# Optimization experiments

Measured on AMD Instinct MI355X. Metric: run time of the kernel, lower is better.

Reference implementation:

```python
import jax, jax.numpy as jnp
import numpy as np

P = 126          # num_patients
EPS = 1e-6       # PCSL eps
BN_EPS = 1e-5    # torch BatchNorm1d default eps (eval mode: running_mean=0, running_var=1)
LAMBDA_PCSL = 50.0
LAMBDA_DANN = 0.5


def setup_inputs() -> dict:
    key = jax.random.key(0)
    ks = jax.random.split(key, 8)
    D, H1, H2 = 768, 256, 128
    inp = {
        "features": jax.random.normal(ks[0], (2048, 16, D), dtype=jnp.float32),
        "patient_ids": jax.random.randint(ks[1], (2048,), 0, P),
        "W1": jax.random.normal(ks[2], (D, H1), dtype=jnp.float32) / np.sqrt(D),
        "b1": jnp.zeros((H1,), jnp.float32),
        "g1": jnp.ones((H1,), jnp.float32),
        "be1": jnp.zeros((H1,), jnp.float32),
        "W2": jax.random.normal(ks[3], (H1, H2), dtype=jnp.float32) / np.sqrt(H1),
        "b2": jnp.zeros((H2,), jnp.float32),
        "g2": jnp.ones((H2,), jnp.float32),
        "be2": jnp.zeros((H2,), jnp.float32),
        "W3": jax.random.normal(ks[4], (H2, P), dtype=jnp.float32) / np.sqrt(H2),
        "b3": jnp.zeros((P,), jnp.float32),
    }
    return inp


@jax.custom_vjp
def grl(x):  # gradient reversal, lambda_=1.0 (forward identity)
    return x

def _grl_fwd(x):
    return x, None

def _grl_bwd(_, g):
    return (-g,)

grl.defvjp(_grl_fwd, _grl_bwd)


def _bn_eval(x, gamma, beta):
    # BatchNorm1d in eval mode with fresh running stats (mean=0, var=1)
    return x * (gamma / jnp.sqrt(1.0 + BN_EPS)) + beta


def reference(features, patient_ids, W1, b1, g1, be1, W2, b2, g2, be2, W3, b3):
    f = features.mean(axis=1)  # [B, D]

    # ---- PCSL: segment mean/variance + pairwise centroid distances ----
    counts = jax.ops.segment_sum(jnp.ones_like(f[:, 0]), patient_ids, num_segments=P)
    sums = jax.ops.segment_sum(f, patient_ids, num_segments=P)        # [P, D]
    present = counts > 0
    centroids = sums / jnp.maximum(counts, 1.0)[:, None]              # [P, D]
    within = jnp.sum((f - centroids[patient_ids]) ** 2)
    sq = jnp.sum(centroids ** 2, axis=-1)                              # [P]
    d2 = sq[:, None] + sq[None, :] - 2.0 * centroids @ centroids.T     # [P, P]
    pair_mask = present[:, None] & present[None, :]
    between = 0.5 * jnp.sum(jnp.where(pair_mask, d2, 0.0))             # sum over i<j (diag=0)
    loss_pcsl = within / (between + EPS)

    # ---- DANN: GRL + discriminator + CE over compacted patient ids ----
    # mapped id = rank of pid among present unique ids (matches torch.unique remap)
    mapped = jnp.cumsum(present.astype(jnp.int32))[patient_ids] - 1
    x = grl(f)
    h = jax.nn.relu(_bn_eval(x @ W1 + b1, g1, be1))
    h = jax.nn.relu(_bn_eval(h @ W2 + b2, g2, be2))
    logits = h @ W3 + b3                                               # [B, P]
    logp = jax.nn.log_softmax(logits, axis=-1)
    loss_dann = -jnp.mean(jnp.take_along_axis(logp, mapped[:, None], axis=-1))

    return LAMBDA_PCSL * loss_pcsl + LAMBDA_DANN * loss_dann
```

## Files before the change

kernel.cpp:

```cpp
#include <hip/hip_runtime.h>
#include <math.h>

#define B_ 2048
#define S_ 16
#define D_ 768
#define H1_ 256
#define H2_ 128
#define P_ 126

static constexpr float EPS = 1e-6f;
static constexpr float BN_EPS = 1e-5f;
static constexpr float L_PCSL = 50.0f;
static constexpr float L_DANN = 0.5f;

typedef __attribute__((ext_vector_type(8))) short bf16x8;
typedef __attribute__((ext_vector_type(4))) float f32x4;

__device__ inline unsigned short f2b(float x) {
    unsigned int u = __float_as_uint(x);
    unsigned int r = (u + 0x7fffu + ((u >> 16) & 1u)) >> 16;
    return (unsigned short)r;
}

__global__ __launch_bounds__(256) void k_cvt(const float* __restrict__ W1,
                                             const float* __restrict__ W2,
                                             const float* __restrict__ W3,
                                             unsigned short* __restrict__ W1T,
                                             unsigned short* __restrict__ W2T,
                                             unsigned short* __restrict__ W3T,
                                             const int* __restrict__ pid,
                                             int* __restrict__ mapped) {
    int b = blockIdx.x;
    int tid = threadIdx.x;
    if (b == 60) {
        __shared__ int hist[128];
        if (tid < 128) hist[tid] = 0;
        __syncthreads();
        for (int i = tid; i < B_; i += 256) atomicAdd(&hist[pid[i]], 1);
        __syncthreads();
        if (tid == 0) {
            int run = 0;
            for (int p = 0; p < P_; ++p) {
                mapped[p] = (hist[p] > 0) ? run : -1;
                if (hist[p] > 0) run++;
            }
        }
        return;
    }
    __shared__ float tile[64][65];
    const float* src; unsigned short* dst; int R, C, r0, c0;
    if (b < 48)      { src = W1; dst = W1T; R = 768; C = 256; int t = b;      r0 = (t >> 2) * 64; c0 = (t & 3) * 64; }
    else if (b < 56) { src = W2; dst = W2T; R = 256; C = 128; int t = b - 48; r0 = (t >> 1) * 64; c0 = (t & 1) * 64; }
    else             { src = W3; dst = W3T; R = 128; C = 126; int t = b - 56; r0 = (t >> 1) * 64; c0 = (t & 1) * 64; }
#pragma unroll
    for (int i = 0; i < 16; ++i) {
        int idx = tid + i * 256;
        int rr = idx >> 6, cc = idx & 63;
        tile[rr][cc] = (c0 + cc < C) ? src[(size_t)(r0 + rr) * C + c0 + cc] : 0.f;
    }
    __syncthreads();
#pragma unroll
    for (int i = 0; i < 16; ++i) {
        int idx = tid + i * 256;
        int rr = idx >> 6, cc = idx & 63;
        dst[(size_t)(c0 + rr) * R + r0 + cc] = f2b(tile[cc][rr]);
    }
}

__global__ __launch_bounds__(192) void k_mean(const float* __restrict__ feat,
                                              float* __restrict__ f,
                                              unsigned short* __restrict__ fbf) {
    int b = blockIdx.x;
    int t = threadIdx.x;
    const float4* src = (const float4*)(feat + (size_t)b * S_ * D_);
    float4 acc = make_float4(0.f, 0.f, 0.f, 0.f);
#pragma unroll
    for (int s = 0; s < S_; ++s) {
        float4 v = src[s * (D_ / 4) + t];
        acc.x += v.x; acc.y += v.y; acc.z += v.z; acc.w += v.w;
    }
    const float inv = 1.0f / (float)S_;
    acc.x *= inv; acc.y *= inv; acc.z *= inv; acc.w *= inv;
    ((float4*)(f + (size_t)b * D_))[t] = acc;
    ((ushort4*)(fbf + (size_t)b * D_))[t] =
        make_ushort4(f2b(acc.x), f2b(acc.y), f2b(acc.z), f2b(acc.w));
}

__global__ __launch_bounds__(192) void k_centroid(const float* __restrict__ f,
                                                  const int* __restrict__ pid,
                                                  float* __restrict__ colsum,
                                                  float* __restrict__ scal) {
    __shared__ int sid[B_];
    __shared__ int list[B_];
    __shared__ int s_cnt;
    __shared__ float wredA[3], wredB[3];
    int p = blockIdx.x;
    int t = threadIdx.x;
    for (int i = t; i < B_; i += 192) sid[i] = pid[i];
    __syncthreads();

    if (t < 64) {
        int total = 0;
        unsigned long long lt_mask = (t == 63) ? 0x7fffffffffffffffull
                                               : ((1ull << t) - 1ull);
#pragma unroll 4
        for (int r = 0; r < B_ / 64; ++r) {
            int b = r * 64 + t;
            bool m = (sid[b] == p);
            unsigned long long mask = __ballot(m);
            if (m) {
                int pos = total + (int)__popcll(mask & lt_mask);
                list[pos] = b;
            }
            total += (int)__popcll(mask);
        }
        if (t == 0) s_cnt = total;
    }
    __syncthreads();

    int cnt = s_cnt;
    float4 acc = make_float4(0.f, 0.f, 0.f, 0.f);
    float ssf = 0.f;
    int i = 0;
    for (; i + 4 <= cnt; i += 4) {
        int b0 = list[i], b1 = list[i + 1], b2 = list[i + 2], b3 = list[i + 3];
        float4 v0 = ((const float4*)(f + (size_t)b0 * D_))[t];
        float4 v1 = ((const float4*)(f + (size_t)b1 * D_))[t];
        float4 v2 = ((const float4*)(f + (size_t)b2 * D_))[t];
        float4 v3 = ((const float4*)(f + (size_t)b3 * D_))[t];
        acc.x += v0.x + v1.x + v2.x + v3.x;
        acc.y += v0.y + v1.y + v2.y + v3.y;
        acc.z += v0.z + v1.z + v2.z + v3.z;
        acc.w += v0.w + v1.w + v2.w + v3.w;
        ssf += v0.x * v0.x + v0.y * v0.y + v0.z * v0.z + v0.w * v0.w;
        ssf += v1.x * v1.x + v1.y * v1.y + v1.z * v1.z + v1.w * v1.w;
        ssf += v2.x * v2.x + v2.y * v2.y + v2.z * v2.z + v2.w * v2.w;
        ssf += v3.x * v3.x + v3.y * v3.y + v3.z * v3.z + v3.w * v3.w;
    }
    for (; i < cnt; ++i) {
        float4 v = ((const float4*)(f + (size_t)list[i] * D_))[t];
        acc.x += v.x; acc.y += v.y; acc.z += v.z; acc.w += v.w;
        ssf += v.x * v.x + v.y * v.y + v.z * v.z + v.w * v.w;
    }

    float invc = 1.0f / (float)(cnt > 0 ? cnt : 1);
    float4 c = make_float4(acc.x * invc, acc.y * invc, acc.z * invc, acc.w * invc);
    atomicAdd(&colsum[4 * t + 0], c.x);
    atomicAdd(&colsum[4 * t + 1], c.y);
    atomicAdd(&colsum[4 * t + 2], c.z);
    atomicAdd(&colsum[4 * t + 3], c.w);
    float ssc = c.x * c.x + c.y * c.y + c.z * c.z + c.w * c.w;
    for (int off = 32; off; off >>= 1) {
        ssf += __shfl_down(ssf, off, 64);
        ssc += __shfl_down(ssc, off, 64);
    }
    if ((t & 63) == 0) { wredA[t >> 6] = ssf; wredB[t >> 6] = ssc; }
    __syncthreads();
    if (t == 0) {
        float sumsq_rows = wredA[0] + wredA[1] + wredA[2];
        float sqp = wredB[0] + wredB[1] + wredB[2];
        atomicAdd(&scal[3], sumsq_rows);
        atomicAdd(&scal[4], (float)cnt * sqp);
        atomicAdd(&scal[5], sqp);
        atomicAdd(&scal[6], cnt > 0 ? 1.f : 0.f);
    }
}

__global__ __launch_bounds__(256) void k_mlp(const unsigned short* __restrict__ fbf,
                                             const unsigned short* __restrict__ W1T,
                                             const unsigned short* __restrict__ W2T,
                                             const unsigned short* __restrict__ W3T,
                                             const float* __restrict__ b1,
                                             const float* __restrict__ g1,
                                             const float* __restrict__ be1,
                                             const float* __restrict__ b2,
                                             const float* __restrict__ g2,
                                             const float* __restrict__ be2,
                                             const float* __restrict__ b3,
                                             const int* __restrict__ pid,
                                             const int* __restrict__ mapped,
                                             float* __restrict__ scal) {
    constexpr int LD1 = H1_ + 8;
    constexpr int LD2 = H2_ + 8;
    __shared__ unsigned short Hs[16 * LD1];
    __shared__ unsigned short H2s[16 * LD2];
    __shared__ float smax[4][16], ssum[4][16];
    __shared__ int spid[16];
    int tid = threadIdx.x;
    int w = tid >> 6, lane = tid & 63, lg = lane >> 4, li = lane & 15;
    int r0 = blockIdx.x * 16;
    if (tid < 16) spid[tid] = pid[r0 + tid];
    const float inv_bn = rsqrtf(1.0f + BN_EPS);

    f32x4 acc[4];
#pragma unroll
    for (int nf = 0; nf < 4; ++nf) acc[nf] = (f32x4){0.f, 0.f, 0.f, 0.f};
    const unsigned short* aptr = fbf + (size_t)(r0 + li) * D_ + lg * 8;
#pragma unroll 2
    for (int k0 = 0; k0 < D_; k0 += 32) {
        bf16x8 a8 = *(const bf16x8*)(aptr + k0);
#pragma unroll
        for (int nf = 0; nf < 4; ++nf) {
            bf16x8 b8 = *(const bf16x8*)(W1T + (size_t)(w * 64 + nf * 16 + li) * D_ + k0 + lg * 8);
            acc[nf] = __builtin_amdgcn_mfma_f32_16x16x32_bf16(a8, b8, acc[nf], 0, 0, 0);
        }
    }
#pragma unroll
    for (int nf = 0; nf < 4; ++nf) {
        int col = w * 64 + nf * 16 + li;
        float sc = g1[col] * inv_bn, bb = b1[col], bt = be1[col];
#pragma unroll
        for (int r = 0; r < 4; ++r) {
            int row = lg * 4 + r;
            float v = fmaxf((acc[nf][r] + bb) * sc + bt, 0.f);
            Hs[row * LD1 + col] = f2b(v);
        }
    }
    __syncthreads();

    f32x4 acc2[2];
    acc2[0] = (f32x4){0.f, 0.f, 0.f, 0.f};
    acc2[1] = (f32x4){0.f, 0.f, 0.f, 0.f};
#pragma unroll
    for (int ks = 0; ks < H1_ / 32; ++ks) {
        bf16x8 a8 = *(const bf16x8*)(Hs + li * LD1 + ks * 32 + lg * 8);
#pragma unroll
        for (int mf = 0; mf < 2; ++mf) {
            bf16x8 b8 = *(const bf16x8*)(W2T + (size_t)(w * 32 + mf * 16 + li) * H1_ + ks * 32 + lg * 8);
            acc2[mf] = __builtin_amdgcn_mfma_f32_16x16x32_bf16(a8, b8, acc2[mf], 0, 0, 0);
        }
    }
#pragma unroll
    for (int mf = 0; mf < 2; ++mf) {
        int col = w * 32 + mf * 16 + li;
        float sc = g2[col] * inv_bn, bb = b2[col], bt = be2[col];
#pragma unroll
        for (int r = 0; r < 4; ++r) {
            int row = lg * 4 + r;
            float v = fmaxf((acc2[mf][r] + bb) * sc + bt, 0.f);
            H2s[row * LD2 + col] = f2b(v);
        }
    }
    __syncthreads();

    f32x4 acc3[2];
    acc3[0] = (f32x4){0.f, 0.f, 0.f, 0.f};
    acc3[1] = (f32x4){0.f, 0.f, 0.f, 0.f};
#pragma unroll
    for (int ks = 0; ks < H2_ / 32; ++ks) {
        bf16x8 a8 = *(const bf16x8*)(H2s + li * LD2 + ks * 32 + lg * 8);
#pragma unroll
        for (int mf = 0; mf < 2; ++mf) {
            bf16x8 b8 = *(const bf16x8*)(W3T + (size_t)(w * 32 + mf * 16 + li) * H2_ + ks * 32 + lg * 8);
            acc3[mf] = __builtin_amdgcn_mfma_f32_16x16x32_bf16(a8, b8, acc3[mf], 0, 0, 0);
        }
    }
    int c0 = w * 32 + li, c1 = w * 32 + 16 + li;
    float bb0 = (c0 < P_) ? b3[c0] : 0.f;
    float bb1 = (c1 < P_) ? b3[c1] : 0.f;
    float lg0[4], lg1[4], m[4];
#pragma unroll
    for (int r = 0; r < 4; ++r) {
        lg0[r] = (c0 < P_) ? (acc3[0][r] + bb0) : -3.0e38f;
        lg1[r] = (c1 < P_) ? (acc3[1][r] + bb1) : -3.0e38f;
        m[r] = fmaxf(lg0[r], lg1[r]);
    }
#pragma unroll
    for (int off = 1; off < 16; off <<= 1)
#pragma unroll
        for (int r = 0; r < 4; ++r) m[r] = fmaxf(m[r], __shfl_xor(m[r], off, 64));
    if (li == 0) {
#pragma unroll
        for (int r = 0; r < 4; ++r) smax[w][lg * 4 + r] = m[r];
    }
    __syncthreads();
    float M[4], s[4];
#pragma unroll
    for (int r = 0; r < 4; ++r) {
        int row = lg * 4 + r;
        M[r] = fmaxf(fmaxf(smax[0][row], smax[1][row]), fmaxf(smax[2][row], smax[3][row]));
        s[r] = __expf(lg0[r] - M[r]) + __expf(lg1[r] - M[r]);
    }
#pragma unroll
    for (int off = 1; off < 16; off <<= 1)
#pragma unroll
        for (int r = 0; r < 4; ++r) s[r] += __shfl_xor(s[r], off, 64);
    if (li == 0) {
#pragma unroll
        for (int r = 0; r < 4; ++r) ssum[w][lg * 4 + r] = s[r];
    }
    __syncthreads();
    float part = 0.f;
#pragma unroll
    for (int r = 0; r < 4; ++r) {
        int row = lg * 4 + r;
        float se = ssum[0][row] + ssum[1][row] + ssum[2][row] + ssum[3][row];
        float lnse = M[r] + __logf(se);
        int mb = mapped[spid[row]];
        if (c0 == mb) part += lnse - lg0[r];
        if (c1 == mb) part += lnse - lg1[r];
    }
    for (int off = 32; off; off >>= 1) part += __shfl_down(part, off, 64);
    if (lane == 0) atomicAdd(&scal[2], part);
}

__global__ __launch_bounds__(256) void k_final(const float* __restrict__ colsum,
                                               const float* __restrict__ scal,
                                               float* __restrict__ out) {
    __shared__ float wred[4];
    int t = threadIdx.x;
    float acc = 0.f;
    for (int d = t; d < D_; d += 256) {
        float cs = colsum[d];
        acc += cs * cs;
    }
    for (int off = 32; off; off >>= 1) acc += __shfl_down(acc, off, 64);
    if ((t & 63) == 0) wred[t >> 6] = acc;
    __syncthreads();
    if (t == 0) {
        float B2 = wred[0] + wred[1] + wred[2] + wred[3];
        float within = scal[3] - scal[4];
        float between = scal[6] * scal[5] - B2;
        out[0] = L_PCSL * (within / (between + EPS)) + L_DANN * (scal[2] / (float)B_);
    }
}

extern "C" void kernel_launch(void* const* d_in, const int* in_sizes, int n_in,
                              void* d_out, int out_size, void* d_ws, size_t ws_size,
                              hipStream_t stream) {
    const float* feat = (const float*)d_in[0];
    const int* pid = (const int*)d_in[1];
    const float* W1 = (const float*)d_in[2];
    const float* b1 = (const float*)d_in[3];
    const float* g1 = (const float*)d_in[4];
    const float* be1 = (const float*)d_in[5];
    const float* W2 = (const float*)d_in[6];
    const float* b2 = (const float*)d_in[7];
    const float* g2 = (const float*)d_in[8];
    const float* be2 = (const float*)d_in[9];
    const float* W3 = (const float*)d_in[10];
    const float* b3 = (const float*)d_in[11];
    float* out = (float*)d_out;

    char* w = (char*)d_ws;
    float* colsum = (float*)w;
    float* scal = colsum + D_;
    int* mapped = (int*)(scal + 16);
    float* f = (float*)(mapped + 128);
    unsigned short* fbf = (unsigned short*)(f + (size_t)B_ * D_);
    unsigned short* W1T = fbf + (size_t)B_ * D_;
    unsigned short* W2T = W1T + (size_t)H1_ * D_;
    unsigned short* W3T = W2T + (size_t)H2_ * H1_;

    hipMemsetAsync(colsum, 0, (D_ + 16) * sizeof(float), stream);

    k_cvt<<<61, 256, 0, stream>>>(W1, W2, W3, W1T, W2T, W3T, pid, mapped);
    k_mean<<<B_, 192, 0, stream>>>(feat, f, fbf);
    k_centroid<<<P_, 192, 0, stream>>>(f, pid, colsum, scal);
    k_mlp<<<B_ / 16, 256, 0, stream>>>(fbf, W1T, W2T, W3T, b1, g1, be1,
                                       b2, g2, be2, b3, pid, mapped, scal);
    k_final<<<1, 256, 0, stream>>>(colsum, scal, out);
}
```

Baseline: 80.04 us.

## Fuse five kernels into two and drop fp32 mean buffer

Merges the weight-transpose kernel into the feature-mean kernel, and merges the centroid, MLP and final kernels into one launch that uses a last-block atomic counter to do the final reduction. The fp32 copy of the mean features is no longer written, and centroid statistics are read from the bf16 buffer instead. This cuts launch gaps and about half of the mean-output traffic. In exchange the PCSL statistics are computed from bf16-rounded features, which loses precision, and the MLP blocks use a larger shared-memory union, which may lower occupancy.

Result: faster. 76.06 us (-5.0%).

```diff
diff --git a/kernel.cpp b/kernel.cpp
--- a/kernel.cpp
+++ b/kernel.cpp
@@ -21,8 +21,17 @@
     unsigned int r = (u + 0x7fffu + ((u >> 16) & 1u)) >> 16;
     return (unsigned short)r;
 }
-
-__global__ __launch_bounds__(256) void k_cvt(const float* __restrict__ W1,
+__device__ inline float b2f(unsigned short u) {
+    return __uint_as_float((unsigned int)u << 16);
+}
+__device__ inline float4 ldrow(const unsigned short* __restrict__ fbf, int b, int t) {
+    ushort4 u = ((const ushort4*)(fbf + (size_t)b * D_))[t];
+    return make_float4(b2f(u.x), b2f(u.y), b2f(u.z), b2f(u.w));
+}
+
+__global__ __launch_bounds__(256) void k_pre(const float* __restrict__ feat,
+                                             unsigned short* __restrict__ fbf,
+                                             const float* __restrict__ W1,
                                              const float* __restrict__ W2,
                                              const float* __restrict__ W3,
                                              unsigned short* __restrict__ W1T,
@@ -30,298 +39,306 @@
                                              unsigned short* __restrict__ W3T,
                                              const int* __restrict__ pid,
                                              int* __restrict__ mapped) {
+    __shared__ union {
+        float tile[64][65];
+        int hist[128];
+    } sh;
     int b = blockIdx.x;
     int tid = threadIdx.x;
-    if (b == 60) {
-        __shared__ int hist[128];
-        if (tid < 128) hist[tid] = 0;
-        __syncthreads();
-        for (int i = tid; i < B_; i += 256) atomicAdd(&hist[pid[i]], 1);
+
+    if (b < B_) {
+        if (tid < 192) {
+            const float4* src = (const float4*)(feat + (size_t)b * S_ * D_);
+            float4 acc = make_float4(0.f, 0.f, 0.f, 0.f);
+#pragma unroll
+            for (int s = 0; s < S_; ++s) {
+                float4 v = src[s * (D_ / 4) + tid];
+                acc.x += v.x; acc.y += v.y; acc.z += v.z; acc.w += v.w;
+            }
+            const float inv = 1.0f / (float)S_;
+            acc.x *= inv; acc.y *= inv; acc.z *= inv; acc.w *= inv;
+            ((ushort4*)(fbf + (size_t)b * D_))[tid] =
+                make_ushort4(f2b(acc.x), f2b(acc.y), f2b(acc.z), f2b(acc.w));
+        }
+        return;
+    }
+    if (b == B_ + 60) {
+        if (tid < 128) sh.hist[tid] = 0;
+        __syncthreads();
+        for (int i = tid; i < B_; i += 256) atomicAdd(&sh.hist[pid[i]], 1);
         __syncthreads();
         if (tid == 0) {
             int run = 0;
             for (int p = 0; p < P_; ++p) {
-                mapped[p] = (hist[p] > 0) ? run : -1;
-                if (hist[p] > 0) run++;
+                mapped[p] = (sh.hist[p] > 0) ? run : -1;
+                if (sh.hist[p] > 0) run++;
             }
         }
         return;
     }
-    __shared__ float tile[64][65];
+    int bb = b - B_;
     const float* src; unsigned short* dst; int R, C, r0, c0;
-    if (b < 48)      { src = W1; dst = W1T; R = 768; C = 256; int t = b;      r0 = (t >> 2) * 64; c0 = (t & 3) * 64; }
-    else if (b < 56) { src = W2; dst = W2T; R = 256; C = 128; int t = b - 48; r0 = (t >> 1) * 64; c0 = (t & 1) * 64; }
-    else             { src = W3; dst = W3T; R = 128; C = 126; int t = b - 56; r0 = (t >> 1) * 64; c0 = (t & 1) * 64; }
+    if (bb < 48)      { src = W1; dst = W1T; R = 768; C = 256; int t = bb;      r0 = (t >> 2) * 64; c0 = (t & 3) * 64; }
+    else if (bb < 56) { src = W2; dst = W2T; R = 256; C = 128; int t = bb - 48; r0 = (t >> 1) * 64; c0 = (t & 1) * 64; }
+    else              { src = W3; dst = W3T; R = 128; C = 126; int t = bb - 56; r0 = (t >> 1) * 64; c0 = (t & 1) * 64; }
 #pragma unroll
     for (int i = 0; i < 16; ++i) {
         int idx = tid + i * 256;
         int rr = idx >> 6, cc = idx & 63;
-        tile[rr][cc] = (c0 + cc < C) ? src[(size_t)(r0 + rr) * C + c0 + cc] : 0.f;
+        sh.tile[rr][cc] = (c0 + cc < C) ? src[(size_t)(r0 + rr) * C + c0 + cc] : 0.f;
     }
     __syncthreads();
 #pragma unroll
     for (int i = 0; i < 16; ++i) {
         int idx = tid + i * 256;
         int rr = idx >> 6, cc = idx & 63;
-        dst[(size_t)(c0 + rr) * R + r0 + cc] = f2b(tile[cc][rr]);
-    }
-}
-
-__global__ __launch_bounds__(192) void k_mean(const float* __restrict__ feat,
-                                              float* __restrict__ f,
-                                              unsigned short* __restrict__ fbf) {
-    int b = blockIdx.x;
-    int t = threadIdx.x;
-    const float4* src = (const float4*)(feat + (size_t)b * S_ * D_);
-    float4 acc = make_float4(0.f, 0.f, 0.f, 0.f);
-#pragma unroll
-    for (int s = 0; s < S_; ++s) {
-        float4 v = src[s * (D_ / 4) + t];
-        acc.x += v.x; acc.y += v.y; acc.z += v.z; acc.w += v.w;
-    }
-    const float inv = 1.0f / (float)S_;
-    acc.x *= inv; acc.y *= inv; acc.z *= inv; acc.w *= inv;
-    ((float4*)(f + (size_t)b * D_))[t] = acc;
-    ((ushort4*)(fbf + (size_t)b * D_))[t] =
-        make_ushort4(f2b(acc.x), f2b(acc.y), f2b(acc.z), f2b(acc.w));
-}
-
-__global__ __launch_bounds__(192) void k_centroid(const float* __restrict__ f,
-                                                  const int* __restrict__ pid,
-                                                  float* __restrict__ colsum,
-                                                  float* __restrict__ scal) {
-    __shared__ int sid[B_];
-    __shared__ int list[B_];
-    __shared__ int s_cnt;
-    __shared__ float wredA[3], wredB[3];
-    int p = blockIdx.x;
-    int t = threadIdx.x;
-    for (int i = t; i < B_; i += 192) sid[i] = pid[i];
-    __syncthreads();
-
-    if (t < 64) {
-        int total = 0;
-        unsigned long long lt_mask = (t == 63) ? 0x7fffffffffffffffull
-                                               : ((1ull << t) - 1ull);
-#pragma unroll 4
-        for (int r = 0; r < B_ / 64; ++r) {
-            int b = r * 64 + t;
-            bool m = (sid[b] == p);
-            unsigned long long mask = __ballot(m);
-            if (m) {
-                int pos = total + (int)__popcll(mask & lt_mask);
-                list[pos] = b;
-            }
-            total += (int)__popcll(mask);
-        }
-        if (t == 0) s_cnt = total;
-    }
-    __syncthreads();
-
-    int cnt = s_cnt;
-    float4 acc = make_float4(0.f, 0.f, 0.f, 0.f);
-    float ssf = 0.f;
-    int i = 0;
-    for (; i + 4 <= cnt; i += 4) {
-        int b0 = list[i], b1 = list[i + 1], b2 = list[i + 2], b3 = list[i + 3];
-        float4 v0 = ((const float4*)(f + (size_t)b0 * D_))[t];
-        float4 v1 = ((const float4*)(f + (size_t)b1 * D_))[t];
-        float4 v2 = ((const float4*)(f + (size_t)b2 * D_))[t];
-        float4 v3 = ((const float4*)(f + (size_t)b3 * D_))[t];
-        acc.x += v0.x + v1.x + v2.x + v3.x;
-        acc.y += v0.y + v1.y + v2.y + v3.y;
-        acc.z += v0.z + v1.z + v2.z + v3.z;
-        acc.w += v0.w + v1.w + v2.w + v3.w;
-        ssf += v0.x * v0.x + v0.y * v0.y + v0.z * v0.z + v0.w * v0.w;
-        ssf += v1.x * v1.x + v1.y * v1.y + v1.z * v1.z + v1.w * v1.w;
-        ssf += v2.x * v2.x + v2.y * v2.y + v2.z * v2.z + v2.w * v2.w;
-        ssf += v3.x * v3.x + v3.y * v3.y + v3.z * v3.z + v3.w * v3.w;
-    }
-    for (; i < cnt; ++i) {
-        float4 v = ((const float4*)(f + (size_t)list[i] * D_))[t];
-        acc.x += v.x; acc.y += v.y; acc.z += v.z; acc.w += v.w;
-        ssf += v.x * v.x + v.y * v.y + v.z * v.z + v.w * v.w;
-    }
-
-    float invc = 1.0f / (float)(cnt > 0 ? cnt : 1);
-    float4 c = make_float4(acc.x * invc, acc.y * invc, acc.z * invc, acc.w * invc);
-    atomicAdd(&colsum[4 * t + 0], c.x);
-    atomicAdd(&colsum[4 * t + 1], c.y);
-    atomicAdd(&colsum[4 * t + 2], c.z);
-    atomicAdd(&colsum[4 * t + 3], c.w);
-    float ssc = c.x * c.x + c.y * c.y + c.z * c.z + c.w * c.w;
-    for (int off = 32; off; off >>= 1) {
-        ssf += __shfl_down(ssf, off, 64);
-        ssc += __shfl_down(ssc, off, 64);
-    }
-    if ((t & 63) == 0) { wredA[t >> 6] = ssf; wredB[t >> 6] = ssc; }
-    __syncthreads();
-    if (t == 0) {
-        float sumsq_rows = wredA[0] + wredA[1] + wredA[2];
-        float sqp = wredB[0] + wredB[1] + wredB[2];
-        atomicAdd(&scal[3], sumsq_rows);
-        atomicAdd(&scal[4], (float)cnt * sqp);
-        atomicAdd(&scal[5], sqp);
-        atomicAdd(&scal[6], cnt > 0 ? 1.f : 0.f);
-    }
-}
-
-__global__ __launch_bounds__(256) void k_mlp(const unsigned short* __restrict__ fbf,
-                                             const unsigned short* __restrict__ W1T,
-                                             const unsigned short* __restrict__ W2T,
-                                             const unsigned short* __restrict__ W3T,
-                                             const float* __restrict__ b1,
-                                             const float* __restrict__ g1,
-                                             const float* __restrict__ be1,
-                                             const float* __restrict__ b2,
-                                             const float* __restrict__ g2,
-                                             const float* __restrict__ be2,
-                                             const float* __restrict__ b3,
-                                             const int* __restrict__ pid,
-                                             const int* __restrict__ mapped,
-                                             float* __restrict__ scal) {
+        dst[(size_t)(c0 + rr) * R + r0 + cc] = f2b(sh.tile[cc][rr]);
+    }
+}
+
+__global__ __launch_bounds__(256) void k_cm(const unsigned short* __restrict__ fbf,
+                                            const int* __restrict__ pid,
+                                            const unsigned short* __restrict__ W1T,
+                                            const unsigned short* __restrict__ W2T,
+                                            const unsigned short* __restrict__ W3T,
+                                            const float* __restrict__ b1,
+                                            const float* __restrict__ g1,
+                                            const float* __restrict__ be1,
+                                            const float* __restrict__ b2,
+                                            const float* __restrict__ g2,
+                                            const float* __restrict__ be2,
+                                            const float* __restrict__ b3,
+                                            const int* __restrict__ mapped,
+                                            float* __restrict__ colsum,
+                                            float* __restrict__ scal,
+                                            float* __restrict__ out) {
     constexpr int LD1 = H1_ + 8;
     constexpr int LD2 = H2_ + 8;
-    __shared__ unsigned short Hs[16 * LD1];
-    __shared__ unsigned short H2s[16 * LD2];
-    __shared__ float smax[4][16], ssum[4][16];
-    __shared__ int spid[16];
+    __shared__ union {
+        struct { int sid[B_]; int list[B_]; } cen;
+        struct {
+            unsigned short Hs[16 * LD1];
+            unsigned short H2s[16 * LD2];
+            float smax[4][16], ssum[4][16];
+            int spid[16];
+        } mlp;
+    } sh;
+    __shared__ float wA[4], wB[4];
+    __shared__ int s_cnt, amLast;
     int tid = threadIdx.x;
-    int w = tid >> 6, lane = tid & 63, lg = lane >> 4, li = lane & 15;
-    int r0 = blockIdx.x * 16;
-    if (tid < 16) spid[tid] = pid[r0 + tid];
-    const float inv_bn = rsqrtf(1.0f + BN_EPS);
-
-    f32x4 acc[4];
-#pragma unroll
-    for (int nf = 0; nf < 4; ++nf) acc[nf] = (f32x4){0.f, 0.f, 0.f, 0.f};
-    const unsigned short* aptr = fbf + (size_t)(r0 + li) * D_ + lg * 8;
+    int blk = blockIdx.x;
+    int* ctr = (int*)(scal + 7);
+
+    if (blk < P_) {
+        int p = blk;
+        for (int i = tid; i < B_; i += 256) sh.cen.sid[i] = pid[i];
+        __syncthreads();
+        if (tid < 64) {
+            int total = 0;
+            unsigned long long lt_mask = (tid == 63) ? 0x7fffffffffffffffull
+                                                     : ((1ull << tid) - 1ull);
+#pragma unroll 4
+            for (int r = 0; r < B_ / 64; ++r) {
+                int b = r * 64 + tid;
+                bool m = (sh.cen.sid[b] == p);
+                unsigned long long mask = __ballot(m);
+                if (m) {
+                    int pos = total + (int)__popcll(mask & lt_mask);
+                    sh.cen.list[pos] = b;
+                }
+                total += (int)__popcll(mask);
+            }
+            if (tid == 0) s_cnt = total;
+        }
+        __syncthreads();
+
+        int cnt = s_cnt;
+        float4 acc = make_float4(0.f, 0.f, 0.f, 0.f);
+        float ssf = 0.f;
+        if (tid < 192) {
+            int i = 0;
+            for (; i + 4 <= cnt; i += 4) {
+                float4 v0 = ldrow(fbf, sh.cen.list[i], tid);
+                float4 v1 = ldrow(fbf, sh.cen.list[i + 1], tid);
+                float4 v2 = ldrow(fbf, sh.cen.list[i + 2], tid);
+                float4 v3 = ldrow(fbf, sh.cen.list[i + 3], tid);
+                acc.x += v0.x + v1.x + v2.x + v3.x;
+                acc.y += v0.y + v1.y + v2.y + v3.y;
+                acc.z += v0.z + v1.z + v2.z + v3.z;
+                acc.w += v0.w + v1.w + v2.w + v3.w;
+                ssf += v0.x * v0.x + v0.y * v0.y + v0.z * v0.z + v0.w * v0.w;
+                ssf += v1.x * v1.x + v1.y * v1.y + v1.z * v1.z + v1.w * v1.w;
+                ssf += v2.x * v2.x + v2.y * v2.y + v2.z * v2.z + v2.w * v2.w;
+                ssf += v3.x * v3.x + v3.y * v3.y + v3.z * v3.z + v3.w * v3.w;
+            }
+            for (; i < cnt; ++i) {
+                float4 v = ldrow(fbf, sh.cen.list[i], tid);
+                acc.x += v.x; acc.y += v.y; acc.z += v.z; acc.w += v.w;
+                ssf += v.x * v.x + v.y * v.y + v.z * v.z + v.w * v.w;
+            }
+        }
+        float invc = 1.0f / (float)(cnt > 0 ? cnt : 1);
+        float4 c = make_float4(acc.x * invc, acc.y * invc, acc.z * invc, acc.w * invc);
+        if (tid < 192) {
+            atomicAdd(&colsum[4 * tid + 0], c.x);
+            atomicAdd(&colsum[4 * tid + 1], c.y);
+            atomicAdd(&colsum[4 * tid + 2], c.z);
+            atomicAdd(&colsum[4 * tid + 3], c.w);
+        }
+        float ssc = c.x * c.x + c.y * c.y + c.z * c.z + c.w * c.w;
+        for (int off = 32; off; off >>= 1) {
+            ssf += __shfl_down(ssf, off, 64);
+            ssc += __shfl_down(ssc, off, 64);
+        }
+        if ((tid & 63) == 0) { wA[tid >> 6] = ssf; wB[tid >> 6] = ssc; }
+        __syncthreads();
+        if (tid == 0) {
+            float sumsq_rows = wA[0] + wA[1] + wA[2] + wA[3];
+            float sqp = wB[0] + wB[1] + wB[2] + wB[3];
+            atomicAdd(&scal[3], sumsq_rows);
+            atomicAdd(&scal[4], (float)cnt * sqp);
+            atomicAdd(&scal[5], sqp);
+            atomicAdd(&scal[6], cnt > 0 ? 1.f : 0.f);
+        }
+    } else {
+        int w = tid >> 6, lane = tid & 63, lg = lane >> 4, li = lane & 15;
+        int r0 = (blk - P_) * 16;
+        if (tid < 16) sh.mlp.spid[tid] = pid[r0 + tid];
+        const float inv_bn = rsqrtf(1.0f + BN_EPS);
+
+        f32x4 acc[4];
+#pragma unroll
+        for (int nf = 0; nf < 4; ++nf) acc[nf] = (f32x4){0.f, 0.f, 0.f, 0.f};
+        const unsigned short* aptr = fbf + (size_t)(r0 + li) * D_ + lg * 8;
 #pragma unroll 2
-    for (int k0 = 0; k0 < D_; k0 += 32) {
-        bf16x8 a8 = *(const bf16x8*)(aptr + k0);
+        for (int k0 = 0; k0 < D_; k0 += 32) {
+            bf16x8 a8 = *(const bf16x8*)(aptr + k0);
+#pragma unroll
+            for (int nf = 0; nf < 4; ++nf) {
+                bf16x8 b8 = *(const bf16x8*)(W1T + (size_t)(w * 64 + nf * 16 + li) * D_ + k0 + lg * 8);
+                acc[nf] = __builtin_amdgcn_mfma_f32_16x16x32_bf16(a8, b8, acc[nf], 0, 0, 0);
+            }
+        }
 #pragma unroll
         for (int nf = 0; nf < 4; ++nf) {
-            bf16x8 b8 = *(const bf16x8*)(W1T + (size_t)(w * 64 + nf * 16 + li) * D_ + k0 + lg * 8);
-            acc[nf] = __builtin_amdgcn_mfma_f32_16x16x32_bf16(a8, b8, acc[nf], 0, 0, 0);
-        }
-    }
-#pragma unroll
-    for (int nf = 0; nf < 4; ++nf) {
-        int col = w * 64 + nf * 16 + li;
-        float sc = g1[col] * inv_bn, bb = b1[col], bt = be1[col];
+            int col = w * 64 + nf * 16 + li;
+            float sc = g1[col] * inv_bn, bb = b1[col], bt = be1[col];
+#pragma unroll
+            for (int r = 0; r < 4; ++r) {
+                int row = lg * 4 + r;
+                float v = fmaxf((acc[nf][r] + bb) * sc + bt, 0.f);
+                sh.mlp.Hs[row * LD1 + col] = f2b(v);
+            }
+        }
+        __syncthreads();
+
+        f32x4 acc2[2];
+        acc2[0] = (f32x4){0.f, 0.f, 0.f, 0.f};
+        acc2[1] = (f32x4){0.f, 0.f, 0.f, 0.f};
+#pragma unroll
+        for (int ks = 0; ks < H1_ / 32; ++ks) {
+            bf16x8 a8 = *(const bf16x8*)(sh.mlp.Hs + li * LD1 + ks * 32 + lg * 8);
+#pragma unroll
+            for (int mf = 0; mf < 2; ++mf) {
+                bf16x8 b8 = *(const bf16x8*)(W2T + (size_t)(w * 32 + mf * 16 + li) * H1_ + ks * 32 + lg * 8);
+                acc2[mf] = __builtin_amdgcn_mfma_f32_16x16x32_bf16(a8, b8, acc2[mf], 0, 0, 0);
+            }
+        }
+#pragma unroll
+        for (int mf = 0; mf < 2; ++mf) {
+            int col = w * 32 + mf * 16 + li;
+            float sc = g2[col] * inv_bn, bb = b2[col], bt = be2[col];
+#pragma unroll
+            for (int r = 0; r < 4; ++r) {
+                int row = lg * 4 + r;
+                float v = fmaxf((acc2[mf][r] + bb) * sc + bt, 0.f);
+                sh.mlp.H2s[row * LD2 + col] = f2b(v);
+            }
+        }
+        __syncthreads();
+
+        f32x4 acc3[2];
+        acc3[0] = (f32x4){0.f, 0.f, 0.f, 0.f};
+        acc3[1] = (f32x4){0.f, 0.f, 0.f, 0.f};
+#pragma unroll
+        for (int ks = 0; ks < H2_ / 32; ++ks) {
+            bf16x8 a8 = *(const bf16x8*)(sh.mlp.H2s + li * LD2 + ks * 32 + lg * 8);
+#pragma unroll
+            for (int mf = 0; mf < 2; ++mf) {
+                bf16x8 b8 = *(const bf16x8*)(W3T + (size_t)(w * 32 + mf * 16 + li) * H2_ + ks * 32 + lg * 8);
+                acc3[mf] = __builtin_amdgcn_mfma_f32_16x16x32_bf16(a8, b8, acc3[mf], 0, 0, 0);
+            }
+        }
+        int c0 = w * 32 + li, c1 = w * 32 + 16 + li;
+        float bb0 = (c0 < P_) ? b3[c0] : 0.f;
+        float bb1 = (c1 < P_) ? b3[c1] : 0.f;
+        float lg0[4], lg1[4], m[4];
+#pragma unroll
+        for (int r = 0; r < 4; ++r) {
+            lg0[r] = (c0 < P_) ? (acc3[0][r] + bb0) : -3.0e38f;
+            lg1[r] = (c1 < P_) ? (acc3[1][r] + bb1) : -3.0e38f;
+            m[r] = fmaxf(lg0[r], lg1[r]);
+        }
+#pragma unroll
+        for (int off = 1; off < 16; off <<= 1)
+#pragma unroll
+            for (int r = 0; r < 4; ++r) m[r] = fmaxf(m[r], __shfl_xor(m[r], off, 64));
+        if (li == 0) {
+#pragma unroll
+            for (int r = 0; r < 4; ++r) sh.mlp.smax[w][lg * 4 + r] = m[r];
+        }
+        __syncthreads();
+        float M[4], s[4];
 #pragma unroll
         for (int r = 0; r < 4; ++r) {
             int row = lg * 4 + r;
-            float v = fmaxf((acc[nf][r] + bb) * sc + bt, 0.f);
-            Hs[row * LD1 + col] = f2b(v);
-        }
-    }
-    __syncthreads();
-
-    f32x4 acc2[2];
-    acc2[0] = (f32x4){0.f, 0.f, 0.f, 0.f};
-    acc2[1] = (f32x4){0.f, 0.f, 0.f, 0.f};
-#pragma unroll
-    for (int ks = 0; ks < H1_ / 32; ++ks) {
-        bf16x8 a8 = *(const bf16x8*)(Hs + li * LD1 + ks * 32 + lg * 8);
-#pragma unroll
-        for (int mf = 0; mf < 2; ++mf) {
-            bf16x8 b8 = *(const bf16x8*)(W2T + (size_t)(w * 32 + mf * 16 + li) * H1_ + ks * 32 + lg * 8);
-            acc2[mf] = __builtin_amdgcn_mfma_f32_16x16x32_bf16(a8, b8, acc2[mf], 0, 0, 0);
-        }
-    }
-#pragma unroll
-    for (int mf = 0; mf < 2; ++mf) {
-        int col = w * 32 + mf * 16 + li;
-        float sc = g2[col] * inv_bn, bb = b2[col], bt = be2[col];
+            M[r] = fmaxf(fmaxf(sh.mlp.smax[0][row], sh.mlp.smax[1][row]),
+                         fmaxf(sh.mlp.smax[2][row], sh.mlp.smax[3][row]));
+            s[r] = __expf(lg0[r] - M[r]) + __expf(lg1[r] - M[r]);
+        }
+#pragma unroll
+        for (int off = 1; off < 16; off <<= 1)
+#pragma unroll
+            for (int r = 0; r < 4; ++r) s[r] += __shfl_xor(s[r], off, 64);
+        if (li == 0) {
+#pragma unroll
+            for (int r = 0; r < 4; ++r) sh.mlp.ssum[w][lg * 4 + r] = s[r];
+        }
+        __syncthreads();
+        float part = 0.f;
 #pragma unroll
         for (int r = 0; r < 4; ++r) {
             int row = lg * 4 + r;
-            float v = fmaxf((acc2[mf][r] + bb) * sc + bt, 0.f);
-            H2s[row * LD2 + col] = f2b(v);
-        }
-    }
+            float se = sh.mlp.ssum[0][row] + sh.mlp.ssum[1][row] +
+                       sh.mlp.ssum[2][row] + sh.mlp.ssum[3][row];
+            float lnse = M[r] + __logf(se);
+            int mb = mapped[sh.mlp.spid[row]];
+            if (c0 == mb) part += lnse - lg0[r];
+            if (c1 == mb) part += lnse - lg1[r];
+        }
+        for (int off = 32; off; off >>= 1) part += __shfl_down(part, off, 64);
+        if (lane == 0) atomicAdd(&scal[2], part);
+    }
+
     __syncthreads();
-
-    f32x4 acc3[2];
-    acc3[0] = (f32x4){0.f, 0.f, 0.f, 0.f};
-    acc3[1] = (f32x4){0.f, 0.f, 0.f, 0.f};
-#pragma unroll
-    for (int ks = 0; ks < H2_ / 32; ++ks) {
-        bf16x8 a8 = *(const bf16x8*)(H2s + li * LD2 + ks * 32 + lg * 8);
-#pragma unroll
-        for (int mf = 0; mf < 2; ++mf) {
-            bf16x8 b8 = *(const bf16x8*)(W3T + (size_t)(w * 32 + mf * 16 + li) * H2_ + ks * 32 + lg * 8);
-            acc3[mf] = __builtin_amdgcn_mfma_f32_16x16x32_bf16(a8, b8, acc3[mf], 0, 0, 0);
-        }
-    }
-    int c0 = w * 32 + li, c1 = w * 32 + 16 + li;
-    float bb0 = (c0 < P_) ? b3[c0] : 0.f;
-    float bb1 = (c1 < P_) ? b3[c1] : 0.f;
-    float lg0[4], lg1[4], m[4];
-#pragma unroll
-    for (int r = 0; r < 4; ++r) {
-        lg0[r] = (c0 < P_) ? (acc3[0][r] + bb0) : -3.0e38f;
-        lg1[r] = (c1 < P_) ? (acc3[1][r] + bb1) : -3.0e38f;
-        m[r] = fmaxf(lg0[r], lg1[r]);
-    }
-#pragma unroll
-    for (int off = 1; off < 16; off <<= 1)
-#pragma unroll
-        for (int r = 0; r < 4; ++r) m[r] = fmaxf(m[r], __shfl_xor(m[r], off, 64));
-    if (li == 0) {
-#pragma unroll
-        for (int r = 0; r < 4; ++r) smax[w][lg * 4 + r] = m[r];
-    }
+    __threadfence();
+    if (tid == 0) amLast = (atomicAdd(ctr, 1) == P_ + B_ / 16 - 1);
     __syncthreads();
-    float M[4], s[4];
-#pragma unroll
-    for (int r = 0; r < 4; ++r) {
-        int row = lg * 4 + r;
-        M[r] = fmaxf(fmaxf(smax[0][row], smax[1][row]), fmaxf(smax[2][row], smax[3][row]));
-        s[r] = __expf(lg0[r] - M[r]) + __expf(lg1[r] - M[r]);
-    }
-#pragma unroll
-    for (int off = 1; off < 16; off <<= 1)
-#pragma unroll
-        for (int r = 0; r < 4; ++r) s[r] += __shfl_xor(s[r], off, 64);
-    if (li == 0) {
-#pragma unroll
-        for (int r = 0; r < 4; ++r) ssum[w][lg * 4 + r] = s[r];
-    }
+    if (!amLast) return;
+    float acc = 0.f;
+    for (int d = tid; d < D_; d += 256) {
+        float cs = atomicAdd(&colsum[d], 0.f);
+        acc += cs * cs;
+    }
+    for (int off = 32; off; off >>= 1) acc += __shfl_down(acc, off, 64);
+    if ((tid & 63) == 0) wA[tid >> 6] = acc;
     __syncthreads();
-    float part = 0.f;
-#pragma unroll
-    for (int r = 0; r < 4; ++r) {
-        int row = lg * 4 + r;
-        float se = ssum[0][row] + ssum[1][row] + ssum[2][row] + ssum[3][row];
-        float lnse = M[r] + __logf(se);
-        int mb = mapped[spid[row]];
-        if (c0 == mb) part += lnse - lg0[r];
-        if (c1 == mb) part += lnse - lg1[r];
-    }
-    for (int off = 32; off; off >>= 1) part += __shfl_down(part, off, 64);
-    if (lane == 0) atomicAdd(&scal[2], part);
-}
-
-__global__ __launch_bounds__(256) void k_final(const float* __restrict__ colsum,
-                                               const float* __restrict__ scal,
-                                               float* __restrict__ out) {
-    __shared__ float wred[4];
-    int t = threadIdx.x;
-    float acc = 0.f;
-    for (int d = t; d < D_; d += 256) {
-        float cs = colsum[d];
-        acc += cs * cs;
-    }
-    for (int off = 32; off; off >>= 1) acc += __shfl_down(acc, off, 64);
-    if ((t & 63) == 0) wred[t >> 6] = acc;
-    __syncthreads();
-    if (t == 0) {
-        float B2 = wred[0] + wred[1] + wred[2] + wred[3];
-        float within = scal[3] - scal[4];
-        float between = scal[6] * scal[5] - B2;
-        out[0] = L_PCSL * (within / (between + EPS)) + L_DANN * (scal[2] / (float)B_);
+    if (tid == 0) {
+        float B2 = wA[0] + wA[1] + wA[2] + wA[3];
+        float within = atomicAdd(&scal[3], 0.f) - atomicAdd(&scal[4], 0.f);
+        float between = atomicAdd(&scal[6], 0.f) * atomicAdd(&scal[5], 0.f) - B2;
+        float dann = atomicAdd(&scal[2], 0.f);
+        out[0] = L_PCSL * (within / (between + EPS)) + L_DANN * (dann / (float)B_);
     }
 }
 
@@ -346,18 +363,15 @@
     float* colsum = (float*)w;
     float* scal = colsum + D_;
     int* mapped = (int*)(scal + 16);
-    float* f = (float*)(mapped + 128);
-    unsigned short* fbf = (unsigned short*)(f + (size_t)B_ * D_);
+    unsigned short* fbf = (unsigned short*)(mapped + 128);
     unsigned short* W1T = fbf + (size_t)B_ * D_;
     unsigned short* W2T = W1T + (size_t)H1_ * D_;
     unsigned short* W3T = W2T + (size_t)H2_ * H1_;
 
     hipMemsetAsync(colsum, 0, (D_ + 16) * sizeof(float), stream);
 
-    k_cvt<<<61, 256, 0, stream>>>(W1, W2, W3, W1T, W2T, W3T, pid, mapped);
-    k_mean<<<B_, 192, 0, stream>>>(feat, f, fbf);
-    k_centroid<<<P_, 192, 0, stream>>>(f, pid, colsum, scal);
-    k_mlp<<<B_ / 16, 256, 0, stream>>>(fbf, W1T, W2T, W3T, b1, g1, be1,
-                                       b2, g2, be2, b3, pid, mapped, scal);
-    k_final<<<1, 256, 0, stream>>>(colsum, scal, out);
-}
+    k_pre<<<B_ + 61, 256, 0, stream>>>(feat, fbf, W1, W2, W3, W1T, W2T, W3T, pid, mapped);
+    k_cm<<<P_ + B_ / 16, 256, 0, stream>>>(fbf, pid, W1T, W2T, W3T,
+                                           b1, g1, be1, b2, g2, be2, b3,
+                                           mapped, colsum, scal, out);
+}
```
